# Kernel tuning notes

Hardware: AMD Instinct MI355X
Metric: run time of the kernel (lower is better)

Reference implementation:

```python
import jax, jax.numpy as jnp
import numpy as np

N = 100000
E = 1600000
IN, HID, OUT = 64, 128, 64
EPS = 1e-5


def setup_inputs() -> dict:
    key = jax.random.key(0)
    ks = jax.random.split(key, 12)
    def nrm(k, shape, scale=0.05):
        return jax.random.normal(k, shape, dtype=jnp.float32) * scale
    z = lambda *s: jnp.zeros(s, jnp.float32)
    o = lambda *s: jnp.ones(s, jnp.float32)
    return {
        "x": jax.random.normal(ks[0], (N, IN), dtype=jnp.float32),
        "edge_index": jax.random.randint(ks[1], (2, E), 0, N, dtype=jnp.int32),
        "W1": nrm(ks[2], (IN, HID)), "b1": z(HID), "g1": o(HID), "be1": z(HID),
        "W2": nrm(ks[3], (HID, HID)), "b2": z(HID), "g2": o(HID), "be2": z(HID),
        "W3": nrm(ks[4], (HID, OUT)), "b3": z(OUT), "g3": o(OUT), "be3": z(OUT),
        "fc1_w": nrm(ks[5], (OUT, 128)), "fc1_b": z(128),
        "fc2_w": nrm(ks[6], (128, 64)), "fc2_b": z(64),
        "fc3_w": nrm(ks[7], (64, 32)), "fc3_b": z(32),
        "fc4_w": nrm(ks[8], (32, 1)), "fc4_b": z(1),
    }


def reference(x, edge_index, W1, b1, g1, be1, W2, b2, g2, be2, W3, b3, g3, be3,
              fc1_w, fc1_b, fc2_w, fc2_b, fc3_w, fc3_b, fc4_w, fc4_b):
    n = x.shape[0]
    # GCNConv: add self-loops, symmetric normalization (computed once, reused).
    loop = jnp.arange(n, dtype=edge_index.dtype)
    row = jnp.concatenate([edge_index[0], loop])  # source
    col = jnp.concatenate([edge_index[1], loop])  # target (aggregation index)
    deg = jax.ops.segment_sum(jnp.ones_like(col, dtype=x.dtype), col, num_segments=n)
    dinv = jnp.where(deg > 0, jax.lax.rsqrt(deg), 0.0)
    norm = dinv[row] * dinv[col]  # [E+N]

    def gcn(h, W, b):
        h = h @ W                               # [N, d_out]
        msg = h[row] * norm[:, None]            # gather + normalize [E+N, d_out]
        return jax.ops.segment_sum(msg, col, num_segments=n) + b  # scatter-add

    def bn(h, g, be):  # BatchNorm over nodes (training-mode batch stats)
        mu = h.mean(0)
        var = h.var(0)
        return (h - mu) * jax.lax.rsqrt(var + EPS) * g + be

    gelu = lambda v: jax.nn.gelu(v, approximate=False)  # torch F.gelu = exact erf

    h = gelu(bn(gcn(x, W1, b1), g1, be1))
    h = gelu(bn(gcn(h, W2, b2), g2, be2))
    h = gelu(bn(gcn(h, W3, b3), g3, be3))
    h = x + h                                   # residual (out == in channels)
    v = h.mean(0)                               # global mean pool -> [OUT]
    v = gelu(v @ fc1_w + fc1_b)                 # dropout is identity in eval
    v = gelu(v @ fc2_w + fc2_b)
    v = gelu(v @ fc3_w + fc3_b)
    return v @ fc4_w + fc4_b                    # [1]
```

## Files before the change

### kernel.cpp

```cpp
#include <hip/hip_runtime.h>
#include <hip/hip_bf16.h>
#include <hip/hip_fp16.h>
#include <math.h>


typedef _Float16 f16x8 __attribute__((ext_vector_type(8)));
typedef _Float16 f16x4 __attribute__((ext_vector_type(4)));
typedef float f32x4 __attribute__((ext_vector_type(4)));

__device__ __forceinline__ float gelu_f(float x) {
    return 0.5f * x * (1.0f + erff(x * 0.7071067811865476f));
}

__device__ __forceinline__ int wave_incl_scan(int v, int lane) {
#pragma unroll
    for (int off = 1; off < 64; off <<= 1) {
        int t = __shfl_up(v, (unsigned)off, 64);
        if (lane >= off) v += t;
    }
    return v;
}

__device__ __forceinline__ void load8h(const __half* __restrict__ p, float* f) {
    uint4 u = *(const uint4*)p;
    const __half2* h2p = (const __half2*)&u;
#pragma unroll
    for (int i = 0; i < 4; i++) {
        float2 t = __half22float2(h2p[i]);
        f[2 * i] = t.x;
        f[2 * i + 1] = t.y;
    }
}

__device__ __forceinline__ void acc8h(const uint4& u, float* f) {
    const __half2* h2p = (const __half2*)&u;
#pragma unroll
    for (int i = 0; i < 4; i++) {
        float2 t = __half22float2(h2p[i]);
        f[2 * i] += t.x;
        f[2 * i + 1] += t.y;
    }
}

__global__ void init_kernel(double* __restrict__ dbls, int ndbl, int* __restrict__ bucketCnt) {
    int i = blockIdx.x * 256 + threadIdx.x;
    if (i < ndbl) dbls[i] = 0.0;
    if (i < 512) bucketCnt[i] = 0;
}

#define EPB 8192
__global__ __launch_bounds__(512) void coarse_count_kernel(const int* __restrict__ col,
                                                           int* __restrict__ bucketCnt,
                                                           int E, int nbuckets) {
    __shared__ int cnt[512];
    for (int b = threadIdx.x; b < nbuckets; b += 512) cnt[b] = 0;
    __syncthreads();
    int e0 = blockIdx.x * EPB;
    int eend = e0 + EPB;
    if (eend > E) eend = E;
    for (int e = e0 + threadIdx.x; e < eend; e += 512)
        atomicAdd(&cnt[col[e] >> 8], 1);
    __syncthreads();
    for (int b = threadIdx.x; b < nbuckets; b += 512) {
        int c = cnt[b];
        if (c) atomicAdd(&bucketCnt[b], c);
    }
}

__global__ __launch_bounds__(512) void bucket_scan_kernel(const int* __restrict__ bucketCnt,
                                                          int* __restrict__ bucketBase,
                                                          int* __restrict__ bcur,
                                                          int nbuckets, int E) {
    int lane = threadIdx.x & 63;
    int wid = threadIdx.x >> 6;
    int v = (threadIdx.x < nbuckets) ? bucketCnt[threadIdx.x] : 0;
    int incl = wave_incl_scan(v, lane);
    __shared__ int ws[8];
    if (lane == 63) ws[wid] = incl;
    __syncthreads();
    if (threadIdx.x == 0) {
        int a = 0;
#pragma unroll
        for (int j = 0; j < 8; j++) { int t = ws[j]; ws[j] = a; a += t; }
    }
    __syncthreads();
    int excl = incl - v + ws[wid];
    if (threadIdx.x < nbuckets) {
        bucketBase[threadIdx.x] = excl;
        bcur[threadIdx.x] = excl;
    }
    if (threadIdx.x == 0) bucketBase[nbuckets] = E;
}

__global__ __launch_bounds__(512) void binstage_kernel(const int* __restrict__ row,
                                                       const int* __restrict__ col,
                                                       int* __restrict__ bcur,
                                                       unsigned int* __restrict__ stage,
                                                       int E, int nbuckets) {
    __shared__ int cnt[512];
    __shared__ int gbase[512];
    int e0 = blockIdx.x * EPB;
    int eend = e0 + EPB;
    if (eend > E) eend = E;
    for (int b = threadIdx.x; b < nbuckets; b += 512) cnt[b] = 0;
    __syncthreads();
    for (int e = e0 + threadIdx.x; e < eend; e += 512)
        atomicAdd(&cnt[col[e] >> 8], 1);
    __syncthreads();
    for (int b = threadIdx.x; b < nbuckets; b += 512) {
        int c = cnt[b];
        gbase[b] = c ? atomicAdd(&bcur[b], c) : 0;
        cnt[b] = 0;
    }
    __syncthreads();
    for (int e = e0 + threadIdx.x; e < eend; e += 512) {
        int c = col[e];
        int b = c >> 8;
        int lp = atomicAdd(&cnt[b], 1);
        stage[gbase[b] + lp] = ((unsigned int)row[e] << 8) | (unsigned int)(c & 255);
    }
}

__global__ __launch_bounds__(256) void bucket_finalize_kernel(const unsigned int* __restrict__ stage,
                                                              const int* __restrict__ bucketBase,
                                                              float* __restrict__ deg,
                                                              float* __restrict__ dinv,
                                                              int* __restrict__ offs,
                                                              int* __restrict__ csr,
                                                              int N) {
    __shared__ int cnt[256];
    __shared__ int loc[256];
    __shared__ int ws[4];
    int b = blockIdx.x;
    int nb0 = b << 8;
    int base = bucketBase[b];
    int end = bucketBase[b + 1];
    cnt[threadIdx.x] = 0;
    __syncthreads();
    int m = end - base;
    for (int t = threadIdx.x; t < m; t += 256)
        atomicAdd(&cnt[stage[base + t] & 255], 1);
    __syncthreads();
    int c = cnt[threadIdx.x];
    int lane = threadIdx.x & 63;
    int wid = threadIdx.x >> 6;
    int incl = wave_incl_scan(c, lane);
    if (lane == 63) ws[wid] = incl;
    __syncthreads();
    if (threadIdx.x == 0) {
        int a = 0;
#pragma unroll
        for (int j = 0; j < 4; j++) { int t = ws[j]; ws[j] = a; a += t; }
    }
    __syncthreads();
    int excl = incl - c + ws[wid];
    int node = nb0 + threadIdx.x;
    if (node < N) {
        float d = (float)(c + 1);
        deg[node] = d;
        dinv[node] = 1.0f / sqrtf(d);
        offs[node] = base + excl;
    }
    loc[threadIdx.x] = excl;
    __syncthreads();
    for (int t = threadIdx.x; t < m; t += 256) {
        unsigned int v = stage[base + t];
        int lc = v & 255;
        int src = (int)(v >> 8);
        int pos = atomicAdd(&loc[lc], 1);
        csr[base + pos] = src;
    }
}

__global__ __launch_bounds__(256) void halfconv_kernel(const float* __restrict__ x,
                                                       const float* __restrict__ dinv,
                                                       __half* __restrict__ xh, int N) {
    int t = blockIdx.x * 256 + threadIdx.x;
    if (t >= N * 8) return;
    int node = t >> 3;
    float dv = dinv[node];
    const float4* p = (const float4*)(x + (size_t)t * 8);
    float4 a = p[0], b = p[1];
    __half2 h[4];
    h[0] = __floats2half2_rn(a.x * dv, a.y * dv);
    h[1] = __floats2half2_rn(a.z * dv, a.w * dv);
    h[2] = __floats2half2_rn(b.x * dv, b.y * dv);
    h[3] = __floats2half2_rn(b.z * dv, b.w * dv);
    *(uint4*)(xh + (size_t)t * 8) = *(uint4*)h;
}

template <int DIN, int DOUT>
__global__ void wconv_kernel(const float* __restrict__ W, _Float16* __restrict__ Wf) {
    int i = blockIdx.x * 256 + threadIdx.x;
    if (i >= DIN * DOUT) return;
    int k = i / DOUT, col = i - k * DOUT;
    int s = k >> 5, krem = k & 31;
    int lg = krem >> 3, j = krem & 7;
    int t = col >> 4, c = col & 15;
    constexpr int NT = DOUT / 16;
    int l = lg * 16 + c;
    Wf[((size_t)(s * NT + t) * 64 + l) * 8 + j] = (_Float16)W[(size_t)k * DOUT + col];
}

template <int D, bool STATS, bool BIAS>
__global__ __launch_bounds__(256) void agg_kernel(const __half* __restrict__ Ut,
                                                  const int* __restrict__ csr,
                                                  const int* __restrict__ offs,
                                                  const float* __restrict__ deg,
                                                  const float* __restrict__ dinv,
                                                  const float* __restrict__ bias,
                                                  float* __restrict__ H,
                                                  double* __restrict__ tmp, int n) {
    constexpr int GPN = D / 8;
    constexpr int NPB = 256 / GPN;
    int g = threadIdx.x / GPN;
    int cl = threadIdx.x % GPN;
    int node = blockIdx.x * NPB + g;
    bool act = node < n;

    float a[8], b[8];
#pragma unroll
    for (int c = 0; c < 8; c++) { a[c] = 0.f; b[c] = 0.f; }

    int start = 0, cnt = 0;
    float dvi = 0.f;
    if (act) {
        start = offs[node];
        cnt = (int)deg[node] - 1;
        dvi = dinv[node];
        load8h(Ut + (size_t)node * D + cl * 8, a);
    }
    const __half* __restrict__ base = Ut + cl * 8;
    int j = 0;
    for (; j + 4 <= cnt; j += 4) {
        int s0 = csr[start + j];
        int s1 = csr[start + j + 1];
        int s2 = csr[start + j + 2];
        int s3 = csr[start + j + 3];
        uint4 u0 = *(const uint4*)(base + (size_t)s0 * D);
        uint4 u1 = *(const uint4*)(base + (size_t)s1 * D);
        uint4 u2 = *(const uint4*)(base + (size_t)s2 * D);
        uint4 u3 = *(const uint4*)(base + (size_t)s3 * D);
        acc8h(u0, a);
        acc8h(u1, b);
        acc8h(u2, a);
        acc8h(u3, b);
    }
    if (j + 2 <= cnt) {
        int s0 = csr[start + j];
        int s1 = csr[start + j + 1];
        uint4 u0 = *(const uint4*)(base + (size_t)s0 * D);
        uint4 u1 = *(const uint4*)(base + (size_t)s1 * D);
        acc8h(u0, a);
        acc8h(u1, b);
        j += 2;
    }
    if (j < cnt) {
        int s0 = csr[start + j];
        uint4 u0 = *(const uint4*)(base + (size_t)s0 * D);
        acc8h(u0, a);
    }

    float h[8];
#pragma unroll
    for (int c = 0; c < 8; c++) h[c] = (a[c] + b[c]) * dvi;
    if (BIAS) {
#pragma unroll
        for (int c = 0; c < 8; c++) h[c] += bias[cl * 8 + c];
    }
    if (act) {
        float* dst = H + (size_t)node * D + cl * 8;
        *(float4*)dst = make_float4(h[0], h[1], h[2], h[3]);
        *(float4*)(dst + 4) = make_float4(h[4], h[5], h[6], h[7]);
    } else {
#pragma unroll
        for (int c = 0; c < 8; c++) h[c] = 0.f;
    }

    if constexpr (STATS) {
        float s[8], q[8];
#pragma unroll
        for (int c = 0; c < 8; c++) { s[c] = h[c]; q[c] = h[c] * h[c]; }
#pragma unroll
        for (int m = GPN; m < 64; m <<= 1) {
#pragma unroll
            for (int c = 0; c < 8; c++) {
                s[c] += __shfl_xor(s[c], m, 64);
                q[c] += __shfl_xor(q[c], m, 64);
            }
        }
        __shared__ float ps[4][GPN][8], pq[4][GPN][8];
        int wid = threadIdx.x >> 6;
        int lane = threadIdx.x & 63;
        if (lane < GPN) {
#pragma unroll
            for (int c = 0; c < 8; c++) { ps[wid][lane][c] = s[c]; pq[wid][lane][c] = q[c]; }
        }
        __syncthreads();
        if (threadIdx.x < D) {
            int cgi = threadIdx.x >> 3, ci = threadIdx.x & 7;
            float t1 = ps[0][cgi][ci] + ps[1][cgi][ci] + ps[2][cgi][ci] + ps[3][cgi][ci];
            float t2 = pq[0][cgi][ci] + pq[1][cgi][ci] + pq[2][cgi][ci] + pq[3][cgi][ci];
            int cp = (blockIdx.x & 63) * 2 * D;
            atomicAdd(&tmp[cp + threadIdx.x], (double)t1);
            atomicAdd(&tmp[cp + D + threadIdx.x], (double)t2);
        }
    }
}

template <int DIN, int DOUT, bool BNIN, bool BIAS, bool DINVOUT, bool HALFOUT, bool STATS>
__global__ __launch_bounds__(256) void mgemm_kernel(const float* __restrict__ Hin,
                                                    const _Float16* __restrict__ Wf,
                                                    const float* __restrict__ scale,
                                                    const float* __restrict__ shift,
                                                    const float* __restrict__ bias,
                                                    const float* __restrict__ dinv,
                                                    void* __restrict__ Out,
                                                    double* __restrict__ tmp, int n) {
    constexpr int NT = DOUT / 16;
    constexpr int NS = DIN / 32;
    constexpr int DP = DIN + 8;
    __shared__ _Float16 Hs[64 * DP];

    int node0 = blockIdx.x * 64;
    int nv = n - node0;
    if (nv > 64) nv = 64;

    constexpr int C4R = DIN / 4;
    for (int f = threadIdx.x; f < 64 * C4R; f += 256) {
        int nn = f / C4R, k4 = f - nn * C4R;
        float4 v = make_float4(0.f, 0.f, 0.f, 0.f);
        if (nn < nv)
            v = *(const float4*)(Hin + (size_t)(node0 + nn) * DIN + k4 * 4);
        if (BNIN) {
            float4 sc = *(const float4*)(scale + k4 * 4);
            float4 sh = *(const float4*)(shift + k4 * 4);
            v.x = gelu_f(fmaf(v.x, sc.x, sh.x));
            v.y = gelu_f(fmaf(v.y, sc.y, sh.y));
            v.z = gelu_f(fmaf(v.z, sc.z, sh.z));
            v.w = gelu_f(fmaf(v.w, sc.w, sh.w));
        }
        f16x4 h;
        h[0] = (_Float16)v.x; h[1] = (_Float16)v.y;
        h[2] = (_Float16)v.z; h[3] = (_Float16)v.w;
        *(f16x4*)(&Hs[nn * DP + k4 * 4]) = h;
    }
    __syncthreads();

    int wv = threadIdx.x >> 6;
    int l = threadIdx.x & 63;
    int arow = l & 15, agrp = l >> 4;

    f32x4 acc[NT];
#pragma unroll
    for (int t = 0; t < NT; t++) acc[t] = (f32x4){0.f, 0.f, 0.f, 0.f};

    const _Float16* hrow = &Hs[(wv * 16 + arow) * DP];
#pragma unroll
    for (int s = 0; s < NS; s++) {
        f16x8 a = *(const f16x8*)(hrow + s * 32 + agrp * 8);
        const _Float16* wb = Wf + (size_t)s * NT * 512 + l * 8;
#pragma unroll
        for (int t = 0; t < NT; t++) {
            f16x8 b = *(const f16x8*)(wb + (size_t)t * 512);
            acc[t] = __builtin_amdgcn_mfma_f32_16x16x32_f16(a, b, acc[t], 0, 0, 0);
        }
    }

    int rbase = wv * 16 + agrp * 4;
    float dv4[4] = {1.f, 1.f, 1.f, 1.f};
    if (DINVOUT) {
#pragma unroll
        for (int r = 0; r < 4; r++)
            if (rbase + r < nv) dv4[r] = dinv[node0 + rbase + r];
    }
    float sa[NT], qa[NT];
#pragma unroll
    for (int t = 0; t < NT; t++) {
        int col = t * 16 + arow;
        float bcol = BIAS ? bias[col] : 0.f;
        float ssum = 0.f, qsum = 0.f;
#pragma unroll
        for (int r = 0; r < 4; r++) {
            int nn = rbase + r;
            bool valid = nn < nv;
            float v = acc[t][r];
            if (DINVOUT) v *= dv4[r];
            v += bcol;
            v = valid ? v : 0.f;
            if (valid) {
                size_t oi = (size_t)(node0 + nn) * DOUT + col;
                if (HALFOUT) ((__half*)Out)[oi] = __float2half(v);
                else ((float*)Out)[oi] = v;
            }
            ssum += v;
            qsum += v * v;
        }
        sa[t] = ssum;
        qa[t] = qsum;
    }

    if constexpr (STATS) {
        __shared__ float ps[4][DOUT], pq[4][DOUT];
#pragma unroll
        for (int t = 0; t < NT; t++) {
            float s = sa[t], q = qa[t];
            s += __shfl_xor(s, 16, 64); q += __shfl_xor(q, 16, 64);
            s += __shfl_xor(s, 32, 64); q += __shfl_xor(q, 32, 64);
            if (l < 16) { ps[wv][t * 16 + l] = s; pq[wv][t * 16 + l] = q; }
        }
        __syncthreads();
        if (threadIdx.x < DOUT) {
            float t1 = ps[0][threadIdx.x] + ps[1][threadIdx.x] +
                       ps[2][threadIdx.x] + ps[3][threadIdx.x];
            float t2 = pq[0][threadIdx.x] + pq[1][threadIdx.x] +
                       pq[2][threadIdx.x] + pq[3][threadIdx.x];
            int cp = (blockIdx.x & 63) * 2 * DOUT;
            atomicAdd(&tmp[cp + threadIdx.x], (double)t1);
            atomicAdd(&tmp[cp + DOUT + threadIdx.x], (double)t2);
        }
    }
}

template <int D>
__global__ void finalize_tmp_kernel(const double* __restrict__ tmp,
                                    const float* __restrict__ g, const float* __restrict__ be,
                                    float* __restrict__ scale, float* __restrict__ shift, int n) {
    int c = threadIdx.x;
    if (c < D) {
        double s = 0.0, q = 0.0;
        for (int gg = 0; gg < 64; gg++) {
            s += tmp[gg * 2 * D + c];
            q += tmp[gg * 2 * D + D + c];
        }
        double mu = s / n;
        double var = q / n - mu * mu;
        double inv = 1.0 / sqrt(var + 1e-5);
        double sc = (double)g[c] * inv;
        scale[c] = (float)sc;
        shift[c] = (float)((double)be[c] - mu * sc);
    }
}

template <int D>
__global__ void combine_kernel(const double* __restrict__ tmp, double* __restrict__ stats) {
    int t = threadIdx.x;
    if (t < 2 * D) {
        double s = 0.0;
        for (int gg = 0; gg < 64; gg++) s += tmp[gg * 2 * D + t];
        stats[t] = s;
    }
}

__global__ __launch_bounds__(256) void norm_pool_kernel(const float* __restrict__ X3,
                                                        const float* __restrict__ x0,
                                                        const double* __restrict__ stats,
                                                        const float* __restrict__ gw,
                                                        const float* __restrict__ be,
                                                        double* __restrict__ pool, int n) {
    constexpr int D = 64;
    constexpr int RPB = 4;
    int c = threadIdx.x % D;
    double mu = stats[c] / n;
    double var = stats[c + D] / n - mu * mu;
    double inv = 1.0 / sqrt(var + 1e-5);
    float scale = (float)((double)gw[c] * inv);
    float shift = (float)((double)be[c] - mu * (double)gw[c] * inv);
    int r0 = threadIdx.x / D;
    int rowsPerGrid = gridDim.x * RPB;
    double s = 0.0;
    for (int r = blockIdx.x * RPB + r0; r < n; r += rowsPerGrid) {
        size_t idx = (size_t)r * D + c;
        float t = fmaf(X3[idx], scale, shift);
        float res = x0[idx] + gelu_f(t);
        s += res;
    }
    __shared__ double sh[256];
    sh[threadIdx.x] = s;
    __syncthreads();
    if (threadIdx.x < D) {
#pragma unroll
        for (int j = 1; j < RPB; j++) s += sh[threadIdx.x + j * D];
        atomicAdd(&pool[c], s);
    }
}

__global__ __launch_bounds__(128) void mlp_kernel(const double* __restrict__ pool,
                                                  const float* __restrict__ w1, const float* __restrict__ b1,
                                                  const float* __restrict__ w2, const float* __restrict__ b2,
                                                  const float* __restrict__ w3, const float* __restrict__ b3,
                                                  const float* __restrict__ w4, const float* __restrict__ b4,
                                                  float* __restrict__ out, int n) {
    __shared__ float v0[64], h1[128], h2[64], h3[32];
    int t = threadIdx.x;
    if (t < 64) v0[t] = (float)(pool[t] / (double)n);
    __syncthreads();
    if (t < 128) {
        float a = b1[t];
        for (int k = 0; k < 64; k++) a = fmaf(v0[k], w1[k * 128 + t], a);
        h1[t] = gelu_f(a);
    }
    __syncthreads();
    if (t < 64) {
        float a = b2[t];
        for (int k = 0; k < 128; k++) a = fmaf(h1[k], w2[k * 64 + t], a);
        h2[t] = gelu_f(a);
    }
    __syncthreads();
    if (t < 32) {
        float a = b3[t];
        for (int k = 0; k < 64; k++) a = fmaf(h2[k], w3[k * 32 + t], a);
        h3[t] = gelu_f(a);
    }
    __syncthreads();
    if (t == 0) {
        float a = b4[0];
        for (int k = 0; k < 32; k++) a = fmaf(h3[k], w4[k], a);
        out[0] = a;
    }
}

extern "C" void kernel_launch(void* const* d_in, const int* in_sizes, int n_in,
                              void* d_out, int out_size, void* d_ws, size_t ws_size,
                              hipStream_t stream) {
    const float* x    = (const float*)d_in[0];
    const int*   ei   = (const int*)d_in[1];
    const float* W1   = (const float*)d_in[2];
    const float* b1   = (const float*)d_in[3];
    const float* g1   = (const float*)d_in[4];
    const float* be1  = (const float*)d_in[5];
    const float* W2   = (const float*)d_in[6];
    const float* b2   = (const float*)d_in[7];
    const float* g2   = (const float*)d_in[8];
    const float* be2  = (const float*)d_in[9];
    const float* W3   = (const float*)d_in[10];
    const float* b3   = (const float*)d_in[11];
    const float* g3   = (const float*)d_in[12];
    const float* be3  = (const float*)d_in[13];
    const float* fc1w = (const float*)d_in[14];
    const float* fc1b = (const float*)d_in[15];
    const float* fc2w = (const float*)d_in[16];
    const float* fc2b = (const float*)d_in[17];
    const float* fc3w = (const float*)d_in[18];
    const float* fc3b = (const float*)d_in[19];
    const float* fc4w = (const float*)d_in[20];
    const float* fc4b = (const float*)d_in[21];

    const int N = in_sizes[0] / 64;
    const int E = in_sizes[1] / 2;
    const int* e_row = ei;
    const int* e_col = ei + E;
    const int nbuckets = (N + 255) >> 8;

    char* ws = (char*)d_ws;
    size_t off = 0;
    double* pool   = (double*)(ws + off); off += 64 * sizeof(double);
    double* tmp1   = (double*)(ws + off); off += 64 * 256 * sizeof(double);
    double* tmp2   = (double*)(ws + off); off += 64 * 256 * sizeof(double);
    double* tmp3   = (double*)(ws + off); off += 64 * 128 * sizeof(double);
    double* stats3 = (double*)(ws + off); off += 128 * sizeof(double);
    const int NDBL = 64 + 64 * 256 * 2 + 64 * 128 + 128;
    float* scale1 = (float*)(ws + off); off += 128 * sizeof(float);
    float* shift1 = (float*)(ws + off); off += 128 * sizeof(float);
    float* scale2 = (float*)(ws + off); off += 128 * sizeof(float);
    float* shift2 = (float*)(ws + off); off += 128 * sizeof(float);
    _Float16* Wf1 = (_Float16*)(ws + off); off += 64 * 128 * sizeof(_Float16);
    _Float16* Wf2 = (_Float16*)(ws + off); off += 128 * 128 * sizeof(_Float16);
    _Float16* Wf3 = (_Float16*)(ws + off); off += 128 * 64 * sizeof(_Float16);
    float* deg   = (float*)(ws + off); off += (size_t)N * sizeof(float);
    float* dinv  = (float*)(ws + off); off += (size_t)N * sizeof(float);
    off = (off + 15) & ~(size_t)15;
    int* offs       = (int*)(ws + off); off += (size_t)N * sizeof(int);
    int* bucketCnt  = (int*)(ws + off); off += 512 * sizeof(int);
    int* bucketBase = (int*)(ws + off); off += 520 * sizeof(int);
    int* bcur       = (int*)(ws + off); off += 512 * sizeof(int);
    int* csr     = (int*)(ws + off); off += (size_t)E * sizeof(int);
    unsigned int* stage = (unsigned int*)(ws + off); off += (size_t)E * sizeof(unsigned int);
    off = (off + 255) & ~(size_t)255;
    __half* Ut   = (__half*)(ws + off); off += (size_t)N * 128 * sizeof(__half);
    float* A1    = (float*)(ws + off);  off += (size_t)N * 64 * sizeof(float);
    float* H     = (float*)(ws + off);  off += (size_t)N * 128 * sizeof(float);
    __half* xh   = Ut;

    const int nb256 = (N + 255) / 256;
    const int eblk = (E + EPB - 1) / EPB;
    const int gblk = (N + 63) / 64;

    init_kernel<<<nb256, 256, 0, stream>>>(pool, NDBL, bucketCnt);
    coarse_count_kernel<<<eblk, 512, 0, stream>>>(e_col, bucketCnt, E, nbuckets);
    bucket_scan_kernel<<<1, 512, 0, stream>>>(bucketCnt, bucketBase, bcur, nbuckets, E);
    binstage_kernel<<<eblk, 512, 0, stream>>>(e_row, e_col, bcur, stage, E, nbuckets);
    bucket_finalize_kernel<<<nbuckets, 256, 0, stream>>>(stage, bucketBase, deg, dinv,
                                                         offs, csr, N);

    wconv_kernel<64, 128><<<32, 256, 0, stream>>>(W1, Wf1);
    wconv_kernel<128, 128><<<64, 256, 0, stream>>>(W2, Wf2);
    wconv_kernel<128, 64><<<32, 256, 0, stream>>>(W3, Wf3);

    halfconv_kernel<<<(N * 8 + 255) / 256, 256, 0, stream>>>(x, dinv, xh, N);
    agg_kernel<64, false, false><<<(N + 31) / 32, 256, 0, stream>>>(
        xh, csr, offs, deg, dinv, nullptr, A1, nullptr, N);
    mgemm_kernel<64, 128, false, true, false, false, true><<<gblk, 256, 0, stream>>>(
        A1, Wf1, nullptr, nullptr, b1, nullptr, H, tmp1, N);
    finalize_tmp_kernel<128><<<1, 128, 0, stream>>>(tmp1, g1, be1, scale1, shift1, N);

    mgemm_kernel<128, 128, true, false, true, true, false><<<gblk, 256, 0, stream>>>(
        H, Wf2, scale1, shift1, nullptr, dinv, Ut, nullptr, N);
    agg_kernel<128, true, true><<<(N + 15) / 16, 256, 0, stream>>>(
        Ut, csr, offs, deg, dinv, b2, H, tmp2, N);
    finalize_tmp_kernel<128><<<1, 128, 0, stream>>>(tmp2, g2, be2, scale2, shift2, N);

    mgemm_kernel<128, 64, true, false, true, true, false><<<gblk, 256, 0, stream>>>(
        H, Wf3, scale2, shift2, nullptr, dinv, Ut, nullptr, N);
    agg_kernel<64, true, true><<<(N + 31) / 32, 256, 0, stream>>>(
        Ut, csr, offs, deg, dinv, b3, H, tmp3, N);
    combine_kernel<64><<<1, 128, 0, stream>>>(tmp3, stats3);

    norm_pool_kernel<<<1024, 256, 0, stream>>>(H, x, stats3, g3, be3, pool, N);
    mlp_kernel<<<1, 128, 0, stream>>>(pool, fc1w, fc1b, fc2w, fc2b, fc3w, fc3b,
                                      fc4w, fc4b, (float*)d_out, N);
}
```

Before: 319.1 us.

## Store intermediate activations in fp16 and vectorize norm-pool over channel groups

Changes the intermediate activation buffers (A1, H) between the aggregation, GEMM and pool kernels from fp32 to fp16. This halves the bytes written and read for these N×128 and N×64 tensors. Loaders now read 8 halves per thread, and norm_pool processes 8 channels per thread with 16-byte loads. The cost is extra rounding on pre-BatchNorm activations, while statistics are still accumulated in fp32/fp64 from the unrounded values.

```diff
diff --git a/kernel.cpp b/kernel.cpp
--- a/kernel.cpp
+++ b/kernel.cpp
@@ -40,6 +40,13 @@
         f[2 * i] += t.x;
         f[2 * i + 1] += t.y;
     }
+}
+
+__device__ __forceinline__ uint4 pack8h(const float* f) {
+    __half2 h[4];
+#pragma unroll
+    for (int i = 0; i < 4; i++) h[i] = __floats2half2_rn(f[2 * i], f[2 * i + 1]);
+    return *(uint4*)h;
 }
 
 __global__ void init_kernel(double* __restrict__ dbls, int ndbl, int* __restrict__ bucketCnt) {
@@ -209,7 +216,7 @@
                                                   const float* __restrict__ deg,
                                                   const float* __restrict__ dinv,
                                                   const float* __restrict__ bias,
-                                                  float* __restrict__ H,
+                                                  __half* __restrict__ H,
                                                   double* __restrict__ tmp, int n) {
     constexpr int GPN = D / 8;
     constexpr int NPB = 256 / GPN;
@@ -269,9 +276,7 @@
         for (int c = 0; c < 8; c++) h[c] += bias[cl * 8 + c];
     }
     if (act) {
-        float* dst = H + (size_t)node * D + cl * 8;
-        *(float4*)dst = make_float4(h[0], h[1], h[2], h[3]);
-        *(float4*)(dst + 4) = make_float4(h[4], h[5], h[6], h[7]);
+        *(uint4*)(H + (size_t)node * D + cl * 8) = pack8h(h);
     } else {
 #pragma unroll
         for (int c = 0; c < 8; c++) h[c] = 0.f;
@@ -309,7 +314,7 @@
 }
 
 template <int DIN, int DOUT, bool BNIN, bool BIAS, bool DINVOUT, bool HALFOUT, bool STATS>
-__global__ __launch_bounds__(256) void mgemm_kernel(const float* __restrict__ Hin,
+__global__ __launch_bounds__(256) void mgemm_kernel(const __half* __restrict__ Hin,
                                                     const _Float16* __restrict__ Wf,
                                                     const float* __restrict__ scale,
                                                     const float* __restrict__ shift,
@@ -326,24 +331,34 @@
     int nv = n - node0;
     if (nv > 64) nv = 64;
 
-    constexpr int C4R = DIN / 4;
-    for (int f = threadIdx.x; f < 64 * C4R; f += 256) {
-        int nn = f / C4R, k4 = f - nn * C4R;
-        float4 v = make_float4(0.f, 0.f, 0.f, 0.f);
-        if (nn < nv)
-            v = *(const float4*)(Hin + (size_t)(node0 + nn) * DIN + k4 * 4);
-        if (BNIN) {
-            float4 sc = *(const float4*)(scale + k4 * 4);
-            float4 sh = *(const float4*)(shift + k4 * 4);
-            v.x = gelu_f(fmaf(v.x, sc.x, sh.x));
-            v.y = gelu_f(fmaf(v.y, sc.y, sh.y));
-            v.z = gelu_f(fmaf(v.z, sc.z, sh.z));
-            v.w = gelu_f(fmaf(v.w, sc.w, sh.w));
-        }
-        f16x4 h;
-        h[0] = (_Float16)v.x; h[1] = (_Float16)v.y;
-        h[2] = (_Float16)v.z; h[3] = (_Float16)v.w;
-        *(f16x4*)(&Hs[nn * DP + k4 * 4]) = h;
+    constexpr int C8R = DIN / 8;
+    for (int f = threadIdx.x; f < 64 * C8R; f += 256) {
+        int nn = f / C8R, k8 = f - nn * C8R;
+        float v[8];
+        if (nn < nv) {
+            load8h(Hin + (size_t)(node0 + nn) * DIN + k8 * 8, v);
+        } else {
+#pragma unroll
+            for (int c = 0; c < 8; c++) v[c] = 0.f;
+        }
+        if (BNIN && nn < nv) {
+            float4 sc0 = *(const float4*)(scale + k8 * 8);
+            float4 sc1 = *(const float4*)(scale + k8 * 8 + 4);
+            float4 sh0 = *(const float4*)(shift + k8 * 8);
+            float4 sh1 = *(const float4*)(shift + k8 * 8 + 4);
+            v[0] = gelu_f(fmaf(v[0], sc0.x, sh0.x));
+            v[1] = gelu_f(fmaf(v[1], sc0.y, sh0.y));
+            v[2] = gelu_f(fmaf(v[2], sc0.z, sh0.z));
+            v[3] = gelu_f(fmaf(v[3], sc0.w, sh0.w));
+            v[4] = gelu_f(fmaf(v[4], sc1.x, sh1.x));
+            v[5] = gelu_f(fmaf(v[5], sc1.y, sh1.y));
+            v[6] = gelu_f(fmaf(v[6], sc1.z, sh1.z));
+            v[7] = gelu_f(fmaf(v[7], sc1.w, sh1.w));
+        }
+        f16x8 h;
+#pragma unroll
+        for (int c = 0; c < 8; c++) h[c] = (_Float16)v[c];
+        *(f16x8*)(&Hs[nn * DP + k8 * 8]) = h;
     }
     __syncthreads();
 
@@ -391,7 +406,7 @@
             if (valid) {
                 size_t oi = (size_t)(node0 + nn) * DOUT + col;
                 if (HALFOUT) ((__half*)Out)[oi] = __float2half(v);
-                else ((float*)Out)[oi] = v;
+                else ((__half*)Out)[oi] = __float2half(v);
             }
             ssum += v;
             qsum += v * v;
@@ -452,7 +467,7 @@
     }
 }
 
-__global__ __launch_bounds__(256) void norm_pool_kernel(const float* __restrict__ X3,
+__global__ __launch_bounds__(256) void norm_pool_kernel(const __half* __restrict__ X3,
                                                         const float* __restrict__ x0,
                                                         const double* __restrict__ stats,
                                                         const float* __restrict__ gw,
@@ -460,28 +475,50 @@
                                                         double* __restrict__ pool, int n) {
     constexpr int D = 64;
     constexpr int RPB = 4;
-    int c = threadIdx.x % D;
-    double mu = stats[c] / n;
-    double var = stats[c + D] / n - mu * mu;
-    double inv = 1.0 / sqrt(var + 1e-5);
-    float scale = (float)((double)gw[c] * inv);
-    float shift = (float)((double)be[c] - mu * (double)gw[c] * inv);
-    int r0 = threadIdx.x / D;
-    int rowsPerGrid = gridDim.x * RPB;
-    double s = 0.0;
-    for (int r = blockIdx.x * RPB + r0; r < n; r += rowsPerGrid) {
-        size_t idx = (size_t)r * D + c;
-        float t = fmaf(X3[idx], scale, shift);
-        float res = x0[idx] + gelu_f(t);
-        s += res;
-    }
-    __shared__ double sh[256];
-    sh[threadIdx.x] = s;
-    __syncthreads();
-    if (threadIdx.x < D) {
-#pragma unroll
-        for (int j = 1; j < RPB; j++) s += sh[threadIdx.x + j * D];
-        atomicAdd(&pool[c], s);
+    int c8 = threadIdx.x & 7;
+    int r0 = threadIdx.x >> 3;
+    float sc[8], sh[8];
+#pragma unroll
+    for (int c = 0; c < 8; c++) {
+        int ch = c8 * 8 + c;
+        double mu = stats[ch] / n;
+        double var = stats[ch + D] / n - mu * mu;
+        double inv = 1.0 / sqrt(var + 1e-5);
+        sc[c] = (float)((double)gw[ch] * inv);
+        sh[c] = (float)((double)be[ch] - mu * (double)gw[ch] * inv);
+    }
+    int rowsPerGrid = gridDim.x * 32;
+    double s[1] = {0.0};
+    float acc[8];
+#pragma unroll
+    for (int c = 0; c < 8; c++) acc[c] = 0.f;
+    double accd[8];
+#pragma unroll
+    for (int c = 0; c < 8; c++) accd[c] = 0.0;
+    for (int r = blockIdx.x * 32 + r0; r < n; r += rowsPerGrid) {
+        float v[8];
+        load8h(X3 + (size_t)r * D + c8 * 8, v);
+        const float4* xp = (const float4*)(x0 + (size_t)r * D + c8 * 8);
+        float4 x0a = xp[0], x0b = xp[1];
+        float xr[8] = {x0a.x, x0a.y, x0a.z, x0a.w, x0b.x, x0b.y, x0b.z, x0b.w};
+#pragma unroll
+        for (int c = 0; c < 8; c++) {
+            float t = fmaf(v[c], sc[c], sh[c]);
+            accd[c] += (double)(xr[c] + gelu_f(t));
+        }
+    }
+    __shared__ double shm[256][8];
+#pragma unroll
+    for (int c = 0; c < 8; c++) shm[threadIdx.x][c] = accd[c];
+    __syncthreads();
+    if (threadIdx.x < 8) {
+        int cg = threadIdx.x;
+#pragma unroll
+        for (int c = 0; c < 8; c++) {
+            double t = 0.0;
+            for (int rr = 0; rr < 32; rr++) t += shm[rr * 8 + cg][c];
+            atomicAdd(&pool[cg * 8 + c], t);
+        }
     }
 }
 
@@ -578,8 +615,8 @@
     unsigned int* stage = (unsigned int*)(ws + off); off += (size_t)E * sizeof(unsigned int);
     off = (off + 255) & ~(size_t)255;
     __half* Ut   = (__half*)(ws + off); off += (size_t)N * 128 * sizeof(__half);
-    float* A1    = (float*)(ws + off);  off += (size_t)N * 64 * sizeof(float);
-    float* H     = (float*)(ws + off);  off += (size_t)N * 128 * sizeof(float);
+    __half* A1   = (__half*)(ws + off); off += (size_t)N * 64 * sizeof(__half);
+    __half* H    = (__half*)(ws + off); off += (size_t)N * 128 * sizeof(__half);
     __half* xh   = Ut;
 
     const int nb256 = (N + 255) / 256;
@@ -600,7 +637,7 @@
     halfconv_kernel<<<(N * 8 + 255) / 256, 256, 0, stream>>>(x, dinv, xh, N);
     agg_kernel<64, false, false><<<(N + 31) / 32, 256, 0, stream>>>(
         xh, csr, offs, deg, dinv, nullptr, A1, nullptr, N);
-    mgemm_kernel<64, 128, false, true, false, false, true><<<gblk, 256, 0, stream>>>(
+    mgemm_kernel<64, 128, false, true, false, true, true><<<gblk, 256, 0, stream>>>(
         A1, Wf1, nullptr, nullptr, b1, nullptr, H, tmp1, N);
     finalize_tmp_kernel<128><<<1, 128, 0, stream>>>(tmp1, g1, be1, scale1, shift1, N);
 
```

Result: slower. 458.6 us (+43.7%).
